# Kernel optimization log

Measured on AMD Instinct MI355X. Metric: run time of the kernel, lower is better.

The kernel has to match this reference:

```python
import jax, jax.numpy as jnp
import numpy as np


def setup_inputs() -> dict:
    key = jax.random.key(0)
    k1, k2, k3 = jax.random.split(key, 3)
    B, Cin, H, W = 16, 64, 224, 224
    Cout, K = 128, 3
    x = jax.random.normal(k1, (B, Cin, H, W), dtype=jnp.float32)
    # PyTorch Conv2d init: uniform(-bound, bound), bound = 1/sqrt(fan_in)
    fan_in = Cin * K * K
    bound = 1.0 / np.sqrt(fan_in)
    conv_weight = jax.random.uniform(k2, (Cout, Cin, K, K), dtype=jnp.float32,
                                     minval=-bound, maxval=bound)
    conv_bias = jax.random.uniform(k3, (Cout,), dtype=jnp.float32,
                                   minval=-bound, maxval=bound)
    return {"x": x, "conv_weight": conv_weight, "conv_bias": conv_bias}


def reference(x, conv_weight, conv_bias):
    # Conv2d, stride=1, padding=0 (VALID), dilation=1, groups=1
    y = jax.lax.conv_general_dilated(
        x, conv_weight,
        window_strides=(1, 1), padding='VALID',
        dimension_numbers=('NCHW', 'OIHW', 'NCHW'))
    y = y + conv_bias[None, :, None, None]
    # channel-wise min reduction, keep channel dim (output [B,1,H',W'])
    y = jnp.min(y, axis=1, keepdims=True)
    # double tanh
    return jnp.tanh(jnp.tanh(y))
```

## Files before the change

### kernel.cpp

```cpp
#include <hip/hip_runtime.h>
#include <hip/hip_bf16.h>

typedef __bf16 bf16_t;
typedef __bf16 bf16x8 __attribute__((ext_vector_type(8)));
typedef float  f32x4  __attribute__((ext_vector_type(4)));

#define CIN  64
#define COUT 128
#define HH   224
#define WW   224
#define OH   222
#define OW   222
#define XT_RS 72

__global__ void prepack_w(const float* __restrict__ w, bf16_t* __restrict__ wpk) {
    int idx = blockIdx.x * 256 + threadIdx.x;
    if (idx >= 9 * COUT * CIN) return;
    int ci  = idx & 63;
    int co  = (idx >> 6) & 127;
    int off = idx >> 13;
    wpk[idx] = (bf16_t)w[(co * CIN + ci) * 9 + off];
}

__global__ __launch_bounds__(256) void conv_min_tanh(
    const float* __restrict__ x, const float* __restrict__ w,
    const float* __restrict__ bias, const bf16_t* __restrict__ wpk,
    float* __restrict__ out)
{
    __shared__ __align__(16) bf16_t xt[10 * 18 * XT_RS];
    __shared__ __align__(16) bf16_t wl[COUT * XT_RS];
    __shared__ float red[2][8][16];

    const int tid = threadIdx.x;
    const int lane = tid & 63;
    const int wv  = tid >> 6;
    const int wgM = wv >> 1;
    const int wgN = wv & 1;
    const int l15 = lane & 15;
    const int lg  = lane >> 4;

    const int owb = blockIdx.x * 16;
    const int ohb = blockIdx.y * 8;
    const int b   = blockIdx.z;

    const float* xb = x + (size_t)b * (CIN * HH * WW);
    for (int idx = tid; idx < 10 * 18 * CIN; idx += 256) {
        int c  = idx % 18;
        int r  = (idx / 18) % 10;
        int ci = idx / 180;
        int rg = ohb + r; if (rg > HH - 1) rg = HH - 1;
        int cg = owb + c; if (cg > WW - 1) cg = WW - 1;
        xt[(r * 18 + c) * XT_RS + ci] = (bf16_t)xb[(ci * HH + rg) * WW + cg];
    }

    float bias4[4];
#pragma unroll
    for (int ni = 0; ni < 4; ni++) bias4[ni] = bias[wgN * 64 + ni * 16 + l15];

    f32x4 acc[4][4];
#pragma unroll
    for (int mi = 0; mi < 4; mi++)
#pragma unroll
        for (int ni = 0; ni < 4; ni++)
            acc[mi][ni] = (f32x4){0.f, 0.f, 0.f, 0.f};

#pragma unroll
    for (int off = 0; off < 9; off++) {
        __syncthreads();
        {
            const int co = tid >> 1, half = tid & 1;
            if (wpk) {
                const uint4* src = reinterpret_cast<const uint4*>(
                    wpk + (size_t)(off * COUT + co) * CIN + half * 32);
                uint4 v0 = src[0], v1 = src[1], v2 = src[2], v3 = src[3];
                uint4* dst = reinterpret_cast<uint4*>(&wl[co * XT_RS + half * 32]);
                dst[0] = v0; dst[1] = v1; dst[2] = v2; dst[3] = v3;
            } else {
#pragma unroll
                for (int j = 0; j < 32; j++) {
                    int ci = half * 32 + j;
                    wl[co * XT_RS + ci] = (bf16_t)w[(co * CIN + ci) * 9 + off];
                }
            }
        }
        __syncthreads();

        const int kh = off / 3, kw = off % 3;
#pragma unroll
        for (int kk = 0; kk < 2; kk++) {
            bf16x8 af[4], bfr[4];
#pragma unroll
            for (int mi = 0; mi < 4; mi++) {
                int row = wgM * 4 + mi + kh;
                int col = l15 + kw;
                af[mi] = *reinterpret_cast<const bf16x8*>(
                    &xt[(row * 18 + col) * XT_RS + kk * 32 + lg * 8]);
            }
#pragma unroll
            for (int ni = 0; ni < 4; ni++) {
                int co = wgN * 64 + ni * 16 + l15;
                bfr[ni] = *reinterpret_cast<const bf16x8*>(
                    &wl[co * XT_RS + kk * 32 + lg * 8]);
            }
#pragma unroll
            for (int mi = 0; mi < 4; mi++)
#pragma unroll
                for (int ni = 0; ni < 4; ni++)
                    acc[mi][ni] = __builtin_amdgcn_mfma_f32_16x16x32_bf16(
                        af[mi], bfr[ni], acc[mi][ni], 0, 0, 0);
        }
    }

#pragma unroll
    for (int mi = 0; mi < 4; mi++) {
#pragma unroll
        for (int r = 0; r < 4; r++) {
            float v =        acc[mi][0][r] + bias4[0];
            v = fminf(v,     acc[mi][1][r] + bias4[1]);
            v = fminf(v,     acc[mi][2][r] + bias4[2]);
            v = fminf(v,     acc[mi][3][r] + bias4[3]);
            v = fminf(v, __shfl_xor(v, 1));
            v = fminf(v, __shfl_xor(v, 2));
            v = fminf(v, __shfl_xor(v, 4));
            v = fminf(v, __shfl_xor(v, 8));
            if (l15 == 0) red[wgN][wgM * 4 + mi][lg * 4 + r] = v;
        }
    }
    __syncthreads();
    if (tid < 128) {
        int prow = tid >> 4, pcol = tid & 15;
        float v = fminf(red[0][prow][pcol], red[1][prow][pcol]);
        v = tanhf(tanhf(v));
        int oh = ohb + prow, ow = owb + pcol;
        if (oh < OH && ow < OW)
            out[((size_t)b * OH + oh) * OW + ow] = v;
    }
}

extern "C" void kernel_launch(void* const* d_in, const int* in_sizes, int n_in,
                              void* d_out, int out_size, void* d_ws, size_t ws_size,
                              hipStream_t stream) {
    const float* x    = (const float*)d_in[0];
    const float* w    = (const float*)d_in[1];
    const float* bias = (const float*)d_in[2];
    float* out = (float*)d_out;

    bf16_t* wpk = nullptr;
    if (ws_size >= (size_t)(9 * COUT * CIN * 2)) {
        wpk = (bf16_t*)d_ws;
        prepack_w<<<288, 256, 0, stream>>>(w, wpk);
    }
    dim3 grid(14, 28, 16);
    conv_min_tanh<<<grid, 256, 0, stream>>>(x, w, bias, wpk, out);
}
```

Measured before the change: 496.6 us.

## Load weights directly from global into registers, drop LDS weight staging and barriers

```diff
diff --git a/kernel.cpp b/kernel.cpp
--- a/kernel.cpp
+++ b/kernel.cpp
@@ -22,13 +22,12 @@
     wpk[idx] = (bf16_t)w[(co * CIN + ci) * 9 + off];
 }
 
-__global__ __launch_bounds__(256) void conv_min_tanh(
+__global__ __launch_bounds__(256, 4) void conv_min_tanh(
     const float* __restrict__ x, const float* __restrict__ w,
     const float* __restrict__ bias, const bf16_t* __restrict__ wpk,
     float* __restrict__ out)
 {
     __shared__ __align__(16) bf16_t xt[10 * 18 * XT_RS];
-    __shared__ __align__(16) bf16_t wl[COUT * XT_RS];
     __shared__ float red[2][8][16];
 
     const int tid = threadIdx.x;
@@ -44,13 +43,22 @@
     const int b   = blockIdx.z;
 
     const float* xb = x + (size_t)b * (CIN * HH * WW);
-    for (int idx = tid; idx < 10 * 18 * CIN; idx += 256) {
-        int c  = idx % 18;
-        int r  = (idx / 18) % 10;
-        int ci = idx / 180;
+    for (int idx = tid; idx < 9 * 10 * CIN; idx += 256) {
+        int c2 = idx % 9;
+        int r  = (idx / 9) % 10;
+        int ci = idx / 90;
         int rg = ohb + r; if (rg > HH - 1) rg = HH - 1;
-        int cg = owb + c; if (cg > WW - 1) cg = WW - 1;
-        xt[(r * 18 + c) * XT_RS + ci] = (bf16_t)xb[(ci * HH + rg) * WW + cg];
+        int cg = owb + 2 * c2;
+        float2 v;
+        if (cg + 1 <= WW - 1) {
+            v = *reinterpret_cast<const float2*>(&xb[(ci * HH + rg) * WW + cg]);
+        } else {
+            float a = xb[(ci * HH + rg) * WW + (WW - 1)];
+            v = make_float2(a, a);
+        }
+        bf16_t* dst = &xt[(r * 18 + 2 * c2) * XT_RS + ci];
+        dst[0]     = (bf16_t)v.x;
+        dst[XT_RS] = (bf16_t)v.y;
     }
 
     float bias4[4];
@@ -64,31 +72,33 @@
         for (int ni = 0; ni < 4; ni++)
             acc[mi][ni] = (f32x4){0.f, 0.f, 0.f, 0.f};
 
+    __syncthreads();
+
 #pragma unroll
     for (int off = 0; off < 9; off++) {
-        __syncthreads();
-        {
-            const int co = tid >> 1, half = tid & 1;
-            if (wpk) {
-                const uint4* src = reinterpret_cast<const uint4*>(
-                    wpk + (size_t)(off * COUT + co) * CIN + half * 32);
-                uint4 v0 = src[0], v1 = src[1], v2 = src[2], v3 = src[3];
-                uint4* dst = reinterpret_cast<uint4*>(&wl[co * XT_RS + half * 32]);
-                dst[0] = v0; dst[1] = v1; dst[2] = v2; dst[3] = v3;
-            } else {
+        const int kh = off / 3, kw = off % 3;
+
+        bf16x8 bfr[2][4];
 #pragma unroll
-                for (int j = 0; j < 32; j++) {
-                    int ci = half * 32 + j;
-                    wl[co * XT_RS + ci] = (bf16_t)w[(co * CIN + ci) * 9 + off];
+        for (int kk = 0; kk < 2; kk++)
+#pragma unroll
+            for (int ni = 0; ni < 4; ni++) {
+                int co = wgN * 64 + ni * 16 + l15;
+                if (wpk) {
+                    bfr[kk][ni] = *reinterpret_cast<const bf16x8*>(
+                        wpk + (size_t)(off * COUT + co) * CIN + kk * 32 + lg * 8);
+                } else {
+                    bf16x8 t;
+#pragma unroll
+                    for (int j = 0; j < 8; j++)
+                        t[j] = (bf16_t)w[(co * CIN + kk * 32 + lg * 8 + j) * 9 + off];
+                    bfr[kk][ni] = t;
                 }
             }
-        }
-        __syncthreads();
 
-        const int kh = off / 3, kw = off % 3;
 #pragma unroll
         for (int kk = 0; kk < 2; kk++) {
-            bf16x8 af[4], bfr[4];
+            bf16x8 af[4];
 #pragma unroll
             for (int mi = 0; mi < 4; mi++) {
                 int row = wgM * 4 + mi + kh;
@@ -97,17 +107,11 @@
                     &xt[(row * 18 + col) * XT_RS + kk * 32 + lg * 8]);
             }
 #pragma unroll
-            for (int ni = 0; ni < 4; ni++) {
-                int co = wgN * 64 + ni * 16 + l15;
-                bfr[ni] = *reinterpret_cast<const bf16x8*>(
-                    &wl[co * XT_RS + kk * 32 + lg * 8]);
-            }
-#pragma unroll
             for (int mi = 0; mi < 4; mi++)
 #pragma unroll
                 for (int ni = 0; ni < 4; ni++)
                     acc[mi][ni] = __builtin_amdgcn_mfma_f32_16x16x32_bf16(
-                        af[mi], bfr[ni], acc[mi][ni], 0, 0, 0);
+                        af[mi], bfr[kk][ni], acc[mi][ni], 0, 0, 0);
         }
     }
 
```

After: 1.062 ms. 2.14x slower.
